# Kernel tuning notes

Hardware: AMD Instinct MI355X
Metric: run time of the kernel (lower is better)

## Reference

```python
import jax, jax.numpy as jnp
import numpy as np
from jax import lax

D_MODEL = 1024
D_STATE = 128
D_CONV = 4
EXPAND = 2
HEADDIM = 64
D_INNER = EXPAND * D_MODEL          # 2048
NHEADS = D_INNER // HEADDIM         # 32
D_IN_PROJ = 2 * D_INNER + 2 * D_STATE + NHEADS  # 4384 (z, xBC, dt)
CONV_CH = D_INNER + 2 * D_STATE     # 2304
CHUNK = 128
EPS = 1e-5
BATCH, SEQ = 2, 2048


def silu(x):
    return x * jax.nn.sigmoid(x)


def rmsnorm(x, w):
    return x * lax.rsqrt(jnp.mean(x * x, axis=-1, keepdims=True) + EPS) * w


def segsum(a):
    # a: (b,h,c,q) -> (b,h,c,q,q); [i,j] = sum_{j<k<=i} a_k, -inf above diag
    q = a.shape[-1]
    cs = jnp.cumsum(a, axis=-1)
    seg = cs[..., :, None] - cs[..., None, :]
    mask = jnp.tril(jnp.ones((q, q), dtype=bool))
    return jnp.where(mask, seg, -jnp.inf)


def ssd(xh, dt, A, B, C):
    # xh: (b,l,h,p), dt: (b,l,h), A: (h,), B,C: (b,l,n). Chunked SSD scan.
    b, l, h, p = xh.shape
    n = B.shape[-1]
    c = l // CHUNK
    X = (xh * dt[..., None]).reshape(b, c, CHUNK, h, p)
    Adt = (A * dt).reshape(b, c, CHUNK, h).transpose(0, 3, 1, 2)  # (b,h,c,q)
    Bc = B.reshape(b, c, CHUNK, n)
    Cc = C.reshape(b, c, CHUNK, n)
    Acs = jnp.cumsum(Adt, axis=-1)
    L = jnp.exp(segsum(Adt))  # (b,h,c,q,q) causal decay within chunk
    Y_diag = jnp.einsum('bcln,bcsn,bhcls,bcshp->bclhp', Cc, Bc, L, X)
    decay_states = jnp.exp(Acs[..., -1:] - Acs)
    states = jnp.einsum('bcln,bhcl,bclhp->bchpn', Bc, decay_states, X)
    chunk_decay = jnp.exp(Acs[..., -1])  # (b,h,c)

    def step(s, inp):
        st, cd = inp
        return s * cd[:, :, None, None] + st, s

    init = jnp.zeros((b, h, p, n), dtype=xh.dtype)
    _, prev = lax.scan(step, init,
                       (states.transpose(1, 0, 2, 3, 4), chunk_decay.transpose(2, 0, 1)))
    # prev: (c,b,h,p,n) = state at start of each chunk
    Y_off = jnp.einsum('bcln,cbhpn,bhcl->bclhp', Cc, prev, jnp.exp(Acs))
    return (Y_diag + Y_off).reshape(b, l, h, p)


def mamba2(x, in_w, conv_w, conv_b, dt_bias, A_log, D, gnorm_w, out_w):
    b, l, _ = x.shape
    zxbcdt = x @ in_w.T  # (b,l,D_IN_PROJ)
    z = zxbcdt[..., :D_INNER]
    xBC = zxbcdt[..., D_INNER:D_INNER + CONV_CH]
    dt = jax.nn.softplus(zxbcdt[..., D_INNER + CONV_CH:] + dt_bias)  # (b,l,h)
    # causal depthwise conv1d
    xp = jnp.pad(xBC, ((0, 0), (D_CONV - 1, 0), (0, 0)))
    conv = sum(xp[:, k:k + l, :] * conv_w[:, k] for k in range(D_CONV)) + conv_b
    xBC = silu(conv)
    xs = xBC[..., :D_INNER]
    B = xBC[..., D_INNER:D_INNER + D_STATE]
    C = xBC[..., D_INNER + D_STATE:]
    A = -jnp.exp(A_log)
    xh = xs.reshape(b, l, NHEADS, HEADDIM)
    y = ssd(xh, dt, A, B, C) + xh * D[None, None, :, None]
    y = y.reshape(b, l, D_INNER)
    y = rmsnorm(y * silu(z), gnorm_w)  # RMSNormGated
    return y @ out_w.T


def setup_inputs() -> dict:
    key = jax.random.key(0)
    ks = jax.random.split(key, 24)
    d = {}
    d['x'] = jax.random.normal(ks[0], (BATCH, SEQ, D_MODEL), dtype=jnp.float32)
    d['norm_w'] = jnp.ones((D_MODEL,), jnp.float32)
    d['out_w_blk'] = jax.random.normal(ks[1], (D_MODEL, 2 * D_MODEL), jnp.float32) * 0.02
    d['out_b_blk'] = jnp.zeros((D_MODEL,), jnp.float32)
    for i, pfx in enumerate(['f_', 'b_']):
        o = 2 + i * 10
        d[pfx + 'in_w'] = jax.random.normal(ks[o], (D_IN_PROJ, D_MODEL), jnp.float32) * 0.02
        d[pfx + 'conv_w'] = jax.random.normal(ks[o + 1], (CONV_CH, D_CONV), jnp.float32) * 0.2
        d[pfx + 'conv_b'] = jnp.zeros((CONV_CH,), jnp.float32)
        d[pfx + 'dt_bias'] = jax.random.normal(ks[o + 2], (NHEADS,), jnp.float32) * 0.1
        d[pfx + 'A_log'] = jnp.log(jax.random.uniform(ks[o + 3], (NHEADS,), jnp.float32, 1.0, 16.0))
        d[pfx + 'D'] = jnp.ones((NHEADS,), jnp.float32)
        d[pfx + 'gnorm_w'] = jnp.ones((D_INNER,), jnp.float32)
        d[pfx + 'out_w'] = jax.random.normal(ks[o + 4], (D_MODEL, D_INNER), jnp.float32) * 0.02
    return d


def reference(x, norm_w, out_w_blk, out_b_blk,
              f_in_w, f_conv_w, f_conv_b, f_dt_bias, f_A_log, f_D, f_gnorm_w, f_out_w,
              b_in_w, b_conv_w, b_conv_b, b_dt_bias, b_A_log, b_D, b_gnorm_w, b_out_w):
    xn = rmsnorm(x, norm_w)
    y_fwd = mamba2(xn, f_in_w, f_conv_w, f_conv_b, f_dt_bias, f_A_log, f_D, f_gnorm_w, f_out_w)
    y_bwd = jnp.flip(
        mamba2(jnp.flip(xn, axis=1), b_in_w, b_conv_w, b_conv_b, b_dt_bias, b_A_log, b_D, b_gnorm_w, b_out_w),
        axis=1)
    out = jnp.concatenate([y_fwd, y_bwd], axis=-1) @ out_w_blk.T + out_b_blk
    return x + out
```

## Files before the change

### kernel.cpp

```cpp
#include <hip/hip_runtime.h>
#include <hip/hip_bf16.h>
#include <math.h>

#define BATCH 2
#define SEQL 2048
#define T 4096
#define DMODEL 1024
#define DINNER 2048
#define DSTATE 128
#define NH 32
#define HD 64
#define DPROJ2 4352
#define CONVCH 2304
#define NCH 16
#define CHUNK 128
#define EPS 1e-5f

#define N_INW ((size_t)DPROJ2 * DMODEL)
#define N_OUTW ((size_t)DMODEL * DINNER)
#define N_ST ((size_t)BATCH * NCH * NH * HD * DSTATE)

typedef unsigned short u16;
typedef __bf16 bf16x8 __attribute__((ext_vector_type(8)));
typedef float f32x4 __attribute__((ext_vector_type(4)));

__device__ __forceinline__ u16 f2b(float f) {
    union { float f; unsigned u; } v; v.f = f;
    unsigned r = v.u + 0x7fffu + ((v.u >> 16) & 1u);
    return (u16)(r >> 16);
}
__device__ __forceinline__ float b2f(u16 b) {
    union { unsigned u; float f; } v; v.u = ((unsigned)b) << 16;
    return v.f;
}
__device__ __forceinline__ int flipseq(int r) {
    return (r & ~(SEQL - 1)) | ((SEQL - 1) - (r & (SEQL - 1)));
}
__device__ __forceinline__ void gload16(const u16* g, u16* l) {
    __builtin_amdgcn_global_load_lds(
        (const __attribute__((address_space(1))) void*)g,
        (__attribute__((address_space(3))) void*)l, 16, 0, 0);
}

__device__ __forceinline__ float blockReduceSum(float v) {
    __shared__ float red_[4];
    for (int off = 32; off > 0; off >>= 1) v += __shfl_down(v, off);
    int lane = threadIdx.x & 63, wid = threadIdx.x >> 6;
    if (lane == 0) red_[wid] = v;
    __syncthreads();
    if (threadIdx.x == 0) {
        float s = 0.f;
        int nw = blockDim.x >> 6;
        for (int i = 0; i < nw; ++i) s += red_[i];
        red_[0] = s;
    }
    __syncthreads();
    return red_[0];
}

__global__ __launch_bounds__(256) void k_rmsnorm(
    const float* __restrict__ x, const float* __restrict__ w,
    u16* __restrict__ outb)
{
    int row = blockIdx.x;
    const float* xr = x + (size_t)row * DMODEL;
    float ss = 0.f;
    for (int i = threadIdx.x; i < DMODEL; i += 256) { float v = xr[i]; ss += v * v; }
    float tot = blockReduceSum(ss);
    float sc = rsqrtf(tot / DMODEL + EPS);
    for (int i = threadIdx.x; i < DMODEL; i += 256)
        outb[(size_t)row * DMODEL + i] = f2b(xr[i] * sc * w[i]);
}

__global__ void k_f2b_all(
    const float* __restrict__ s0, const float* __restrict__ s1,
    const float* __restrict__ s4,
    u16* __restrict__ d_inwb, u16* __restrict__ d_owbb)
{
    size_t i = ((size_t)blockIdx.x * 256 + threadIdx.x) * 4;
    const float* s; u16* d; size_t off;
    if (i < 2 * N_INW) {
        int dir = i >= N_INW;
        off = i - (size_t)dir * N_INW;
        s = dir ? s1 : s0; d = d_inwb + (size_t)dir * N_INW;
    } else {
        off = i - 2 * N_INW;
        if (off >= N_OUTW) return;
        s = s4; d = d_owbb;
    }
    float4 v = *(const float4*)(s + off);
    ushort4 o;
    o.x = f2b(v.x); o.y = f2b(v.y); o.z = f2b(v.z); o.w = f2b(v.w);
    *(ushort4*)(d + off) = o;
}

__global__ __launch_bounds__(256) void k_tw(
    const float* __restrict__ fw, const float* __restrict__ bw, u16* __restrict__ dst)
{
    int dir = blockIdx.z;
    const float* src = dir ? bw : fw;
    u16* d = dst + (size_t)dir * N_OUTW;
    __shared__ u16 t[64][65];
    int e0 = blockIdx.y * 64, c0 = blockIdx.x * 64;
    for (int i = threadIdx.x; i < 64 * 16; i += 256) {
        int el = i >> 4, c4 = (i & 15) * 4;
        float4 v = *(const float4*)(src + (size_t)(e0 + el) * DINNER + c0 + c4);
        t[c4 + 0][el] = f2b(v.x); t[c4 + 1][el] = f2b(v.y);
        t[c4 + 2][el] = f2b(v.z); t[c4 + 3][el] = f2b(v.w);
    }
    __syncthreads();
    for (int i = threadIdx.x; i < 64 * 16; i += 256) {
        int cl = i >> 4, e4 = (i & 15) * 4;
        ushort4 o;
        o.x = t[cl][e4]; o.y = t[cl][e4 + 1]; o.z = t[cl][e4 + 2]; o.w = t[cl][e4 + 3];
        *(ushort4*)(d + (size_t)(c0 + cl) * DMODEL + e0 + e4) = o;
    }
}

__global__ __launch_bounds__(256, 4) void k_mm_in(
    const u16* __restrict__ A, const u16* __restrict__ W0,
    u16* __restrict__ zb0, u16* __restrict__ xbcraw0)
{
    const int K = DMODEL;
    int dir = blockIdx.z;
    const u16* W = W0 + (size_t)dir * N_INW;
    int m0 = blockIdx.y * 128, n0 = blockIdx.x * 128;

    u16* Cout;
    int ldcc, nbase;
    if (n0 < DINNER) {
        Cout = zb0 + (size_t)dir * T * DINNER;
        ldcc = DINNER;
        nbase = n0;
    } else {
        Cout = xbcraw0 + (size_t)dir * T * CONVCH;
        ldcc = CONVCH;
        nbase = n0 - DINNER;
    }

    __shared__ u16 As[2 * 128 * 32];
    __shared__ u16 Bs[2 * 128 * 32];
    int tid = threadIdx.x;
    int lane = tid & 63;
    int wrow = ((tid >> 6) & 1) * 64, wcol = (tid >> 7) * 64;

    int srow = tid >> 2, skof = (tid & 3) * 8;
    int ar1 = m0 + srow, ar2 = ar1 + 64;
    if (dir) { ar1 = flipseq(ar1); ar2 = flipseq(ar2); }
    const u16* ga1 = A + (size_t)ar1 * K + skof;
    const u16* ga2 = A + (size_t)ar2 * K + skof;
    const u16* gb1 = W + (size_t)(n0 + srow) * K + skof;
    const u16* gb2 = gb1 + (size_t)64 * K;
    u16* la1 = As + tid * 8;
    u16* la2 = As + 2048 + tid * 8;
    u16* lb1 = Bs + tid * 8;
    u16* lb2 = Bs + 2048 + tid * 8;

    int aoff[4], boff[4];
    #pragma unroll
    for (int i = 0; i < 4; ++i) {
        aoff[i] = (wrow + i * 16 + (lane & 15)) * 32 + ((lane >> 4) * 8);
        boff[i] = (wcol + i * 16 + (lane & 15)) * 32 + ((lane >> 4) * 8);
    }

    f32x4 acc[4][4] = {};
    for (int kt = 0; kt < K; kt += 64) {
        gload16(ga1, la1);        gload16(ga2, la2);
        gload16(ga1 + 32, la1 + 4096); gload16(ga2 + 32, la2 + 4096);
        gload16(gb1, lb1);        gload16(gb2, lb2);
        gload16(gb1 + 32, lb1 + 4096); gload16(gb2 + 32, lb2 + 4096);
        ga1 += 64; ga2 += 64; gb1 += 64; gb2 += 64;
        __syncthreads();
        #pragma unroll
        for (int ks = 0; ks < 2; ++ks) {
            bf16x8 af[4], bfv[4];
            #pragma unroll
            for (int i = 0; i < 4; ++i) af[i] = *(const bf16x8*)(As + ks * 4096 + aoff[i]);
            #pragma unroll
            for (int j = 0; j < 4; ++j) bfv[j] = *(const bf16x8*)(Bs + ks * 4096 + boff[j]);
            #pragma unroll
            for (int i = 0; i < 4; ++i)
                #pragma unroll
                for (int j = 0; j < 4; ++j)
                    acc[i][j] = __builtin_amdgcn_mfma_f32_16x16x32_bf16(af[i], bfv[j], acc[i][j], 0, 0, 0);
        }
        __syncthreads();
    }

    int rbase = m0 + wrow + ((lane >> 4) << 2);
    int cbase = nbase + wcol + (lane & 15);
    #pragma unroll
    for (int i = 0; i < 4; ++i)
        #pragma unroll
        for (int j = 0; j < 4; ++j)
            #pragma unroll
            for (int r = 0; r < 4; ++r)
                Cout[(size_t)(rbase + i * 16 + r) * ldcc + cbase + j * 16] = f2b(acc[i][j][r]);
}

__global__ __launch_bounds__(256) void k_mm64(
    const u16* __restrict__ A, size_t astride, int lda,
    const u16* __restrict__ W, size_t wstride, int K,
    u16* __restrict__ Cb, int ldc, int coffStride)
{
    int dir = blockIdx.z;
    A += (size_t)dir * astride;
    W += (size_t)dir * wstride;
    int coff = dir * coffStride;

    __shared__ u16 As[2 * 64 * 32];
    __shared__ u16 Bs[2 * 64 * 32];
    int tid = threadIdx.x;
    int lane = tid & 63;
    int w = tid >> 6;
    int m0 = blockIdx.y * 64, n0 = blockIdx.x * 64;
    int wrow = (w & 1) * 32, wcol = (w >> 1) * 32;

    int srow = tid >> 2, skof = (tid & 3) * 8;
    const u16* ga = A + (size_t)(m0 + srow) * lda + skof;
    const u16* gb = W + (size_t)(n0 + srow) * K + skof;
    u16* la = As + tid * 8;
    u16* lb = Bs + tid * 8;

    int aoff[2], boff[2];
    #pragma unroll
    for (int i = 0; i < 2; ++i) {
        aoff[i] = (wrow + i * 16 + (lane & 15)) * 32 + ((lane >> 4) * 8);
        boff[i] = (wcol + i * 16 + (lane & 15)) * 32 + ((lane >> 4) * 8);
    }

    f32x4 acc[2][2] = {};
    for (int kt = 0; kt < K; kt += 64) {
        gload16(ga, la);      gload16(ga + 32, la + 2048);
        gload16(gb, lb);      gload16(gb + 32, lb + 2048);
        ga += 64; gb += 64;
        __syncthreads();
        #pragma unroll
        for (int ks = 0; ks < 2; ++ks) {
            bf16x8 af[2], bfv[2];
            #pragma unroll
            for (int i = 0; i < 2; ++i) af[i] = *(const bf16x8*)(As + ks * 2048 + aoff[i]);
            #pragma unroll
            for (int j = 0; j < 2; ++j) bfv[j] = *(const bf16x8*)(Bs + ks * 2048 + boff[j]);
            #pragma unroll
            for (int i = 0; i < 2; ++i)
                #pragma unroll
                for (int j = 0; j < 2; ++j)
                    acc[i][j] = __builtin_amdgcn_mfma_f32_16x16x32_bf16(af[i], bfv[j], acc[i][j], 0, 0, 0);
        }
        __syncthreads();
    }

    int rbase = m0 + wrow + ((lane >> 4) << 2);
    int cbase = n0 + wcol + (lane & 15);
    #pragma unroll
    for (int i = 0; i < 2; ++i)
        #pragma unroll
        for (int j = 0; j < 2; ++j)
            #pragma unroll
            for (int r = 0; r < 4; ++r)
                Cb[(size_t)(rbase + i * 16 + r) * ldc + coff + cbase + j * 16] = f2b(acc[i][j][r]);
}

__global__ __launch_bounds__(256) void k_mm_fin(
    const u16* __restrict__ A1, const u16* __restrict__ A2,
    const u16* __restrict__ W,
    float* __restrict__ out, const float* __restrict__ bias,
    const float* __restrict__ resid)
{
    __shared__ u16 As[2 * 64 * 32];
    __shared__ u16 Bs[2 * 64 * 32];
    int tid = threadIdx.x;
    int lane = tid & 63;
    int w = tid >> 6;
    int m0 = blockIdx.y * 64, n0 = blockIdx.x * 64;
    int wrow = (w & 1) * 32, wcol = (w >> 1) * 32;

    int srow = tid >> 2, skof = (tid & 3) * 8;
    const u16* ga1 = A1 + (size_t)(m0 + srow) * DINNER + skof;
    const u16* ga2 = A2 + (size_t)flipseq(m0 + srow) * DINNER + skof;
    const u16* gb = W + (size_t)(n0 + srow) * 4096 + skof;
    u16* la = As + tid * 8;
    u16* lb = Bs + tid * 8;

    int aoff[2], boff[2];
    #pragma unroll
    for (int i = 0; i < 2; ++i) {
        aoff[i] = (wrow + i * 16 + (lane & 15)) * 32 + ((lane >> 4) * 8);
        boff[i] = (wcol + i * 16 + (lane & 15)) * 32 + ((lane >> 4) * 8);
    }

    f32x4 acc[2][2] = {};
    #pragma unroll
    for (int half = 0; half < 2; ++half) {
        const u16* ga = half ? ga2 : ga1;
        for (int kt = 0; kt < DINNER; kt += 64) {
            gload16(ga, la);      gload16(ga + 32, la + 2048);
            gload16(gb, lb);      gload16(gb + 32, lb + 2048);
            ga += 64; gb += 64;
            __syncthreads();
            #pragma unroll
            for (int ks = 0; ks < 2; ++ks) {
                bf16x8 af[2], bfv[2];
                #pragma unroll
                for (int i = 0; i < 2; ++i) af[i] = *(const bf16x8*)(As + ks * 2048 + aoff[i]);
                #pragma unroll
                for (int j = 0; j < 2; ++j) bfv[j] = *(const bf16x8*)(Bs + ks * 2048 + boff[j]);
                #pragma unroll
                for (int i = 0; i < 2; ++i)
                    #pragma unroll
                    for (int j = 0; j < 2; ++j)
                        acc[i][j] = __builtin_amdgcn_mfma_f32_16x16x32_bf16(af[i], bfv[j], acc[i][j], 0, 0, 0);
            }
            __syncthreads();
        }
    }

    int rbase = m0 + wrow + ((lane >> 4) << 2);
    int cbase = n0 + wcol + (lane & 15);
    #pragma unroll
    for (int i = 0; i < 2; ++i)
        #pragma unroll
        for (int j = 0; j < 2; ++j)
            #pragma unroll
            for (int r = 0; r < 4; ++r) {
                int row = rbase + i * 16 + r, col = cbase + j * 16;
                out[(size_t)row * DMODEL + col] =
                    acc[i][j][r] + bias[col] + resid[(size_t)row * DMODEL + col];
            }
}

__global__ __launch_bounds__(256) void k_dt2(
    const u16* __restrict__ xnb,
    const float* __restrict__ inw_f, const float* __restrict__ inw_b,
    const float* __restrict__ dtb_f, const float* __restrict__ dtb_b,
    float* __restrict__ dt)
{
    int dir = blockIdx.z;
    const float* wbase = dir ? inw_b : inw_f;
    const float* dtbia = dir ? dtb_b : dtb_f;
    float* dtp = dt + (size_t)dir * T * NH;

    int r0 = blockIdx.x * 4;
    __shared__ float xs[4][1024];
    int tid = threadIdx.x;
    #pragma unroll
    for (int rr = 0; rr < 4; ++rr) {
        int src = dir ? flipseq(r0 + rr) : (r0 + rr);
        ushort4 v = *(const ushort4*)(xnb + (size_t)src * DMODEL + tid * 4);
        xs[rr][tid * 4 + 0] = b2f(v.x); xs[rr][tid * 4 + 1] = b2f(v.y);
        xs[rr][tid * 4 + 2] = b2f(v.z); xs[rr][tid * 4 + 3] = b2f(v.w);
    }
    __syncthreads();
    int h = tid >> 3, part = tid & 7;
    const float* w = wbase + (size_t)(DPROJ2 + h) * DMODEL;
    float a0 = 0.f, a1 = 0.f, a2 = 0.f, a3 = 0.f;
    for (int kk = 0; kk < 128; ++kk) {
        int k = part + (kk << 3);
        float wv = w[k];
        a0 += xs[0][k] * wv; a1 += xs[1][k] * wv;
        a2 += xs[2][k] * wv; a3 += xs[3][k] * wv;
    }
    #pragma unroll
    for (int off = 4; off > 0; off >>= 1) {
        a0 += __shfl_down(a0, off, 8); a1 += __shfl_down(a1, off, 8);
        a2 += __shfl_down(a2, off, 8); a3 += __shfl_down(a3, off, 8);
    }
    if (part == 0) {
        float bsh = dtbia[h];
        float vv[4] = {a0, a1, a2, a3};
        #pragma unroll
        for (int rr = 0; rr < 4; ++rr) {
            float v = vv[rr] + bsh;
            dtp[(size_t)(r0 + rr) * NH + h] = (v > 20.f) ? v : log1pf(expf(v));
        }
    }
}

__global__ void k_conv(const u16* __restrict__ xraw0,
                       const float* __restrict__ cw_f, const float* __restrict__ cw_b,
                       const float* __restrict__ cb_f, const float* __restrict__ cb_b,
                       const float* __restrict__ dt0,
                       u16* __restrict__ xbcb0, u16* __restrict__ xdtb0)
{
    int dir = blockIdx.z;
    const u16* xraw = xraw0 + (size_t)dir * T * CONVCH;
    const float* cw = dir ? cw_b : cw_f;
    const float* cb = dir ? cb_b : cb_f;
    const float* dt = dt0 + (size_t)dir * T * NH;
    u16* xbcb = xbcb0 + (size_t)dir * T * CONVCH;
    u16* xdtb = xdtb0 + (size_t)dir * T * DINNER;

    int idx = blockIdx.x * blockDim.x + threadIdx.x;
    if (idx >= T * (CONVCH / 8)) return;
    int r = idx / (CONVCH / 8);
    int c8 = (idx - r * (CONVCH / 8)) * 8;
    int t = r & (SEQL - 1);
    int b0 = r - t;
    float4 cwv[8];
    #pragma unroll
    for (int j = 0; j < 8; ++j) cwv[j] = *(const float4*)(cw + (size_t)(c8 + j) * 4);
    float acc[8];
    {
        float4 c0 = *(const float4*)(cb + c8);
        float4 c1 = *(const float4*)(cb + c8 + 4);
        acc[0] = c0.x; acc[1] = c0.y; acc[2] = c0.z; acc[3] = c0.w;
        acc[4] = c1.x; acc[5] = c1.y; acc[6] = c1.z; acc[7] = c1.w;
    }
    #pragma unroll
    for (int k = 0; k < 4; ++k) {
        int tt = t + k - 3;
        if (tt < 0) continue;
        const u16* src = xraw + (size_t)(b0 + tt) * CONVCH + c8;
        ushort4 v0 = *(const ushort4*)src;
        ushort4 v1 = *(const ushort4*)(src + 4);
        float xv[8] = {b2f(v0.x), b2f(v0.y), b2f(v0.z), b2f(v0.w),
                       b2f(v1.x), b2f(v1.y), b2f(v1.z), b2f(v1.w)};
        #pragma unroll
        for (int j = 0; j < 8; ++j) {
            float wv = (k == 0) ? cwv[j].x : (k == 1) ? cwv[j].y : (k == 2) ? cwv[j].z : cwv[j].w;
            acc[j] += xv[j] * wv;
        }
    }
    ushort4 o0, o1;
    float s[8];
    #pragma unroll
    for (int j = 0; j < 8; ++j) s[j] = acc[j] / (1.f + __expf(-acc[j]));
    o0.x = f2b(s[0]); o0.y = f2b(s[1]); o0.z = f2b(s[2]); o0.w = f2b(s[3]);
    o1.x = f2b(s[4]); o1.y = f2b(s[5]); o1.z = f2b(s[6]); o1.w = f2b(s[7]);
    *(ushort4*)(xbcb + (size_t)r * CONVCH + c8) = o0;
    *(ushort4*)(xbcb + (size_t)r * CONVCH + c8 + 4) = o1;
    if (c8 < DINNER) {
        float dv = dt[(size_t)r * NH + (c8 >> 6)];
        ushort4 d0, d1;
        d0.x = f2b(s[0] * dv); d0.y = f2b(s[1] * dv); d0.z = f2b(s[2] * dv); d0.w = f2b(s[3] * dv);
        d1.x = f2b(s[4] * dv); d1.y = f2b(s[5] * dv); d1.z = f2b(s[6] * dv); d1.w = f2b(s[7] * dv);
        *(ushort4*)(xdtb + (size_t)r * DINNER + c8) = d0;
        *(ushort4*)(xdtb + (size_t)r * DINNER + c8 + 4) = d1;
    }
}

__global__ void k_acs(const float* __restrict__ dt0,
                      const float* __restrict__ Alog_f, const float* __restrict__ Alog_b,
                      float* __restrict__ acs0, float* __restrict__ cd0)
{
    int dir = blockIdx.z;
    const float* dt = dt0 + (size_t)dir * T * NH;
    const float* A_log = dir ? Alog_b : Alog_f;
    float* acs = acs0 + (size_t)dir * BATCH * NH * NCH * CHUNK;
    float* cd = cd0 + (size_t)dir * BATCH * NH * NCH;

    int bid = blockIdx.x;
    int c = bid & 15;
    int bh = bid >> 4;
    int h = bh & 31;
    int b = bh >> 5;
    int l = threadIdx.x;
    __shared__ float s[128];
    float Ah = -expf(A_log[h]);
    int r = b * SEQL + c * CHUNK + l;
    s[l] = Ah * dt[(size_t)r * NH + h];
    __syncthreads();
    for (int off = 1; off < 128; off <<= 1) {
        float t = (l >= off) ? s[l - off] : 0.f;
        __syncthreads();
        s[l] += t;
        __syncthreads();
    }
    acs[(size_t)bid * 128 + l] = s[l];
    if (l == 127) cd[bid] = expf(s[127]);
}

#define LDW 136
__global__ __launch_bounds__(256) void k_states(
    const u16* __restrict__ xbcb0, const u16* __restrict__ xdtb0,
    const float* __restrict__ acs0, u16* __restrict__ st0)
{
    int dir = blockIdx.z;
    const u16* xbcb = xbcb0 + (size_t)dir * T * CONVCH;
    const u16* xdtb = xdtb0 + (size_t)dir * T * DINNER;
    const float* acs = acs0 + (size_t)dir * BATCH * NH * NCH * CHUNK;
    u16* st = st0 + (size_t)dir * N_ST;

    __shared__ u16 Bt[128 * LDW];
    __shared__ u16 Xt[64 * LDW];
    __shared__ float acs_s[128];
    __shared__ float dec_s[128];
    int tid = threadIdx.x;
    int lane = tid & 63;
    int w = tid >> 6;
    int h = blockIdx.x & 31;
    int bc = blockIdx.x >> 5;
    int c = bc & 15, b = bc >> 4;
    int row0 = b * SEQL + c * CHUNK;

    if (tid < 128)
        acs_s[tid] = acs[(((size_t)(b * NH + h) * NCH + c) << 7) + tid];
    for (int i = tid; i < 128 * 16; i += 256) {
        int l = i >> 4, pg = (i & 15) * 4;
        ushort4 v = *(const ushort4*)(xdtb + (size_t)(row0 + l) * DINNER + h * HD + pg);
        Xt[(pg + 0) * LDW + l] = v.x; Xt[(pg + 1) * LDW + l] = v.y;
        Xt[(pg + 2) * LDW + l] = v.z; Xt[(pg + 3) * LDW + l] = v.w;
    }
    __syncthreads();
    float a_last = acs_s[127];
    if (tid < 128) dec_s[tid] = __expf(a_last - acs_s[tid]);
    __syncthreads();
    for (int i = tid; i < 128 * 32; i += 256) {
        int l = i >> 5, ng = (i & 31) * 4;
        ushort4 v = *(const ushort4*)(xbcb + (size_t)(row0 + l) * CONVCH + DINNER + ng);
        float d = dec_s[l];
        Bt[(ng + 0) * LDW + l] = f2b(b2f(v.x) * d);
        Bt[(ng + 1) * LDW + l] = f2b(b2f(v.y) * d);
        Bt[(ng + 2) * LDW + l] = f2b(b2f(v.z) * d);
        Bt[(ng + 3) * LDW + l] = f2b(b2f(v.w) * d);
    }
    __syncthreads();
    f32x4 tacc[8] = {};
    for (int kk = 0; kk < 4; ++kk) {
        bf16x8 afs = *(const bf16x8*)(Xt + (w * 16 + (lane & 15)) * LDW
                                      + kk * 32 + (lane >> 4) * 8);
        #pragma unroll
        for (int j = 0; j < 8; ++j) {
            bf16x8 bfs = *(const bf16x8*)(Bt + (j * 16 + (lane & 15)) * LDW
                                          + kk * 32 + (lane >> 4) * 8);
            tacc[j] = __builtin_amdgcn_mfma_f32_16x16x32_bf16(afs, bfs, tacc[j], 0, 0, 0);
        }
    }
    size_t sb = (size_t)blockIdx.x * (HD * DSTATE);
    #pragma unroll
    for (int j = 0; j < 8; ++j)
        #pragma unroll
        for (int r = 0; r < 4; ++r) {
            int p = w * 16 + (lane >> 4) * 4 + r;
            int n = j * 16 + (lane & 15);
            st[sb + (size_t)p * DSTATE + n] = f2b(tacc[j][r]);
        }
}

__global__ void k_scan(u16* __restrict__ st0, const float* __restrict__ cd0)
{
    int i = blockIdx.x * blockDim.x + threadIdx.x;
    if (i >= 2 * BATCH * NH * HD * DSTATE) return;
    int dir = i >> 19;
    int j = i & ((1 << 19) - 1);
    u16* st = st0 + (size_t)dir * N_ST;
    const float* cd = cd0 + (size_t)dir * BATCH * NH * NCH;
    int n = j & 127;
    int rest = j >> 7;
    int p = rest & 63; rest >>= 6;
    int h = rest & 31;
    int b = rest >> 5;
    float s = 0.f;
    for (int c = 0; c < NCH; ++c) {
        size_t idx = ((size_t)((b * NCH + c) * NH + h) * HD + p) * DSTATE + n;
        float v = b2f(st[idx]);
        st[idx] = f2b(s);
        s = s * cd[(b * NH + h) * NCH + c] + v;
    }
}

__global__ __launch_bounds__(256) void k_chunk(
    const u16* __restrict__ xbcb0, const u16* __restrict__ xdtb0,
    const float* __restrict__ acs0, const u16* __restrict__ prev0,
    const float* __restrict__ D_f, const float* __restrict__ D_b,
    u16* __restrict__ y0)
{
    int dir = blockIdx.z;
    const u16* xbcb = xbcb0 + (size_t)dir * T * CONVCH;
    const u16* xdtb = xdtb0 + (size_t)dir * T * DINNER;
    const float* acs = acs0 + (size_t)dir * BATCH * NH * NCH * CHUNK;
    const u16* prev = prev0 + (size_t)dir * N_ST;
    const float* Dp = dir ? D_b : D_f;
    u16* y = y0 + (size_t)dir * T * DINNER;

    __shared__ u16 S0[128 * LDW];
    __shared__ u16 Xt[64 * LDW];
    __shared__ float acs_s[128];
    int tid = threadIdx.x;
    int lane = tid & 63;
    int w = tid >> 6;
    int h = blockIdx.x & 31;
    int bc = blockIdx.x >> 5;
    int c = bc & 15, b = bc >> 4;
    int row0 = b * SEQL + c * CHUNK;

    if (tid < 128)
        acs_s[tid] = acs[(((size_t)(b * NH + h) * NCH + c) << 7) + tid];
    for (int i = tid; i < 128 * 16; i += 256) {
        int s = i >> 4, m8 = (i & 15) * 8;
        *(uint4*)(S0 + s * LDW + m8) =
            *(const uint4*)(xbcb + (size_t)(row0 + s) * CONVCH + DINNER + m8);
    }
    for (int i = tid; i < 128 * 16; i += 256) {
        int l = i >> 4, pg = (i & 15) * 4;
        ushort4 v = *(const ushort4*)(xdtb + (size_t)(row0 + l) * DINNER + h * HD + pg);
        Xt[(pg + 0) * LDW + l] = v.x; Xt[(pg + 1) * LDW + l] = v.y;
        Xt[(pg + 2) * LDW + l] = v.z; Xt[(pg + 3) * LDW + l] = v.w;
    }
    __syncthreads();

    int wrow = (w & 1) * 64, wcol = (w >> 1) * 64;
    const u16* cbase = xbcb + (size_t)row0 * CONVCH + DINNER + DSTATE;
    f32x4 sacc[4][4] = {};
    for (int kk = 0; kk < 4; ++kk) {
        bf16x8 af[4], bfr[4];
        #pragma unroll
        for (int i = 0; i < 4; ++i)
            af[i] = *(const bf16x8*)(cbase + (size_t)(wrow + i * 16 + (lane & 15)) * CONVCH
                                     + kk * 32 + (lane >> 4) * 8);
        #pragma unroll
        for (int j = 0; j < 4; ++j)
            bfr[j] = *(const bf16x8*)(S0 + (wcol + j * 16 + (lane & 15)) * LDW
                                      + kk * 32 + (lane >> 4) * 8);
        #pragma unroll
        for (int i = 0; i < 4; ++i)
            #pragma unroll
            for (int j = 0; j < 4; ++j)
                if (wcol + j * 16 <= wrow + i * 16 + 15)
                    sacc[i][j] = __builtin_amdgcn_mfma_f32_16x16x32_bf16(af[i], bfr[j], sacc[i][j], 0, 0, 0);
    }
    __syncthreads();
    #pragma unroll
    for (int i = 0; i < 4; ++i)
        #pragma unroll
        for (int j = 0; j < 4; ++j) {
            int s = wcol + j * 16 + (lane & 15);
            #pragma unroll
            for (int r = 0; r < 4; ++r) {
                int l = wrow + i * 16 + (lane >> 4) * 4 + r;
                float v = (s <= l) ? sacc[i][j][r] * __expf(acs_s[l] - acs_s[s]) : 0.f;
                S0[l * LDW + s] = f2b(v);
            }
        }
    __syncthreads();
    f32x4 yacc[2][4] = {};
    for (int kk = 0; kk < 4; ++kk) {
        bf16x8 af[2], bfr[4];
        #pragma unroll
        for (int i = 0; i < 2; ++i)
            af[i] = *(const bf16x8*)(S0 + (w * 32 + i * 16 + (lane & 15)) * LDW
                                     + kk * 32 + (lane >> 4) * 8);
        #pragma unroll
        for (int j = 0; j < 4; ++j)
            bfr[j] = *(const bf16x8*)(Xt + (j * 16 + (lane & 15)) * LDW
                                      + kk * 32 + (lane >> 4) * 8);
        #pragma unroll
        for (int i = 0; i < 2; ++i)
            #pragma unroll
            for (int j = 0; j < 4; ++j)
                yacc[i][j] = __builtin_amdgcn_mfma_f32_16x16x32_bf16(af[i], bfr[j], yacc[i][j], 0, 0, 0);
    }
    __syncthreads();
    size_t sb = (size_t)blockIdx.x * (HD * DSTATE);
    for (int i = tid; i < 64 * 16; i += 256) {
        int p = i >> 4, m8 = (i & 15) * 8;
        *(uint4*)(S0 + p * LDW + m8) = *(const uint4*)(prev + sb + (size_t)p * DSTATE + m8);
    }
    __syncthreads();
    f32x4 oacc[2][4] = {};
    for (int kk = 0; kk < 4; ++kk) {
        bf16x8 af[2], bfr[4];
        #pragma unroll
        for (int i = 0; i < 2; ++i)
            af[i] = *(const bf16x8*)(cbase + (size_t)(w * 32 + i * 16 + (lane & 15)) * CONVCH
                                     + kk * 32 + (lane >> 4) * 8);
        #pragma unroll
        for (int j = 0; j < 4; ++j)
            bfr[j] = *(const bf16x8*)(S0 + (j * 16 + (lane & 15)) * LDW
                                      + kk * 32 + (lane >> 4) * 8);
        #pragma unroll
        for (int i = 0; i < 2; ++i)
            #pragma unroll
            for (int j = 0; j < 4; ++j)
                oacc[i][j] = __builtin_amdgcn_mfma_f32_16x16x32_bf16(af[i], bfr[j], oacc[i][j], 0, 0, 0);
    }
    float Dh = Dp[h];
    #pragma unroll
    for (int i = 0; i < 2; ++i)
        #pragma unroll
        for (int j = 0; j < 4; ++j)
            #pragma unroll
            for (int r = 0; r < 4; ++r) {
                int l = w * 32 + i * 16 + (lane >> 4) * 4 + r;
                int p = j * 16 + (lane & 15);
                float val = yacc[i][j][r] + __expf(acs_s[l]) * oacc[i][j][r]
                          + b2f(xbcb[(size_t)(row0 + l) * CONVCH + h * HD + p]) * Dh;
                y[(size_t)(row0 + l) * DINNER + h * HD + p] = f2b(val);
            }
}

__global__ __launch_bounds__(256) void k_gate(
    const u16* __restrict__ y0, const u16* __restrict__ zb0,
    const float* __restrict__ gw_f, const float* __restrict__ gw_b,
    u16* __restrict__ out0)
{
    int dir = blockIdx.z;
    const u16* y = y0 + (size_t)dir * T * DINNER;
    const u16* zb = zb0 + (size_t)dir * T * DINNER;
    const float* gw = dir ? gw_b : gw_f;
    u16* out = out0 + (size_t)dir * T * DINNER;

    int r = blockIdx.x;
    __shared__ float tbuf[DINNER];
    int tid = threadIdx.x;
    float ss = 0.f;
    #pragma unroll
    for (int it = 0; it < 2; ++it) {
        int i = (it * 256 + tid) * 4;
        ushort4 yv = *(const ushort4*)(y + (size_t)r * DINNER + i);
        ushort4 zv = *(const ushort4*)(zb + (size_t)r * DINNER + i);
        float z0 = b2f(zv.x), z1 = b2f(zv.y), z2 = b2f(zv.z), z3 = b2f(zv.w);
        float t0 = b2f(yv.x) * (z0 / (1.f + __expf(-z0)));
        float t1 = b2f(yv.y) * (z1 / (1.f + __expf(-z1)));
        float t2 = b2f(yv.z) * (z2 / (1.f + __expf(-z2)));
        float t3 = b2f(yv.w) * (z3 / (1.f + __expf(-z3)));
        tbuf[i] = t0; tbuf[i + 1] = t1; tbuf[i + 2] = t2; tbuf[i + 3] = t3;
        ss += t0 * t0 + t1 * t1 + t2 * t2 + t3 * t3;
    }
    float tot = blockReduceSum(ss);
    float sc = rsqrtf(tot / DINNER + EPS);
    #pragma unroll
    for (int it = 0; it < 2; ++it) {
        int i = (it * 256 + tid) * 4;
        ushort4 o;
        o.x = f2b(tbuf[i] * sc * gw[i]);
        o.y = f2b(tbuf[i + 1] * sc * gw[i + 1]);
        o.z = f2b(tbuf[i + 2] * sc * gw[i + 2]);
        o.w = f2b(tbuf[i + 3] * sc * gw[i + 3]);
        *(ushort4*)(out + (size_t)r * DINNER + i) = o;
    }
}

extern "C" void kernel_launch(void* const* d_in, const int* in_sizes, int n_in,
                              void* d_out, int out_size, void* d_ws, size_t ws_size,
                              hipStream_t stream)
{
    const float* x         = (const float*)d_in[0];
    const float* norm_w    = (const float*)d_in[1];
    const float* out_w_blk = (const float*)d_in[2];
    const float* out_b_blk = (const float*)d_in[3];
    const float* f_in_w    = (const float*)d_in[4];
    const float* f_conv_w  = (const float*)d_in[5];
    const float* f_conv_b  = (const float*)d_in[6];
    const float* f_dt_bias = (const float*)d_in[7];
    const float* f_A_log   = (const float*)d_in[8];
    const float* f_D       = (const float*)d_in[9];
    const float* f_gnorm_w = (const float*)d_in[10];
    const float* f_out_w   = (const float*)d_in[11];
    const float* b_in_w    = (const float*)d_in[12];
    const float* b_conv_w  = (const float*)d_in[13];
    const float* b_conv_b  = (const float*)d_in[14];
    const float* b_dt_bias = (const float*)d_in[15];
    const float* b_A_log   = (const float*)d_in[16];
    const float* b_D       = (const float*)d_in[17];
    const float* b_gnorm_w = (const float*)d_in[18];
    const float* b_out_w   = (const float*)d_in[19];
    float* out = (float*)d_out;

    char* ws = (char*)d_ws;
    u16*  xnb    = (u16*)ws;   ws += (size_t)T * DMODEL * 2;
    u16*  zb     = (u16*)ws;   ws += (size_t)2 * T * DINNER * 2;
    u16*  xbcraw = (u16*)ws;   ws += (size_t)2 * T * CONVCH * 2;
    u16*  xbcb   = (u16*)ws;   ws += (size_t)2 * T * CONVCH * 2;
    u16*  xdtb   = (u16*)ws;   ws += (size_t)2 * T * DINNER * 2;
    float* dtb   = (float*)ws; ws += (size_t)2 * T * NH * 4;
    float* acs   = (float*)ws; ws += (size_t)2 * BATCH * NH * NCH * CHUNK * 4;
    float* cd    = (float*)ws; ws += (size_t)2 * BATCH * NH * NCH * 4;
    u16*  stb    = (u16*)ws;   ws += (size_t)2 * N_ST * 2;
    u16*  inwb   = (u16*)ws;   ws += (size_t)2 * N_INW * 2;
    u16*  fowT2  = (u16*)ws;   ws += (size_t)2 * N_OUTW * 2;
    u16*  owbb   = (u16*)ws;   ws += (size_t)N_OUTW * 2;
    u16*  yb16  = xbcraw;
    u16*  ybb   = xdtb;
    u16*  Mcomb = xbcb;

    k_rmsnorm<<<T, 256, 0, stream>>>(x, norm_w, xnb);
    {
        size_t tot = 2 * N_INW + N_OUTW;
        int blocks = (int)((tot / 4 + 255) / 256);
        k_f2b_all<<<blocks, 256, 0, stream>>>(f_in_w, b_in_w, out_w_blk, inwb, owbb);
    }
    {
        dim3 g(DINNER / 64, DMODEL / 64, 2);
        k_tw<<<g, 256, 0, stream>>>(f_out_w, b_out_w, fowT2);
    }

    {
        dim3 g(DPROJ2 / 128, T / 128, 2);
        k_mm_in<<<g, 256, 0, stream>>>(xnb, inwb, zb, xbcraw);
    }
    {
        dim3 g(T / 4, 1, 2);
        k_dt2<<<g, 256, 0, stream>>>(xnb, f_in_w, b_in_w, f_dt_bias, b_dt_bias, dtb);
    }
    {
        dim3 g((T * (CONVCH / 8) + 255) / 256, 1, 2);
        k_conv<<<g, 256, 0, stream>>>(xbcraw, f_conv_w, b_conv_w, f_conv_b, b_conv_b,
                                      dtb, xbcb, xdtb);
    }
    {
        dim3 g(BATCH * NH * NCH, 1, 2);
        k_acs<<<g, 128, 0, stream>>>(dtb, f_A_log, b_A_log, acs, cd);
    }
    {
        dim3 g(BATCH * NCH * NH, 1, 2);
        k_states<<<g, 256, 0, stream>>>(xbcb, xdtb, acs, stb);
    }
    k_scan<<<(2 * BATCH * NH * HD * DSTATE) / 256, 256, 0, stream>>>(stb, cd);
    {
        dim3 g(BATCH * NCH * NH, 1, 2);
        k_chunk<<<g, 256, 0, stream>>>(xbcb, xdtb, acs, stb, f_D, b_D, yb16);
    }
    {
        dim3 g(T, 1, 2);
        k_gate<<<g, 256, 0, stream>>>(yb16, zb, f_gnorm_w, b_gnorm_w, ybb);
    }
    {
        dim3 g(DINNER / 64, DMODEL / 64, 2);
        k_mm64<<<g, 256, 0, stream>>>(owbb, (size_t)DMODEL, DINNER,
                                      fowT2, N_OUTW, DMODEL,
                                      Mcomb, 2 * DINNER, DINNER);
    }
    {
        dim3 g(DMODEL / 64, T / 64, 1);
        k_mm_fin<<<g, 256, 0, stream>>>(ybb, ybb + (size_t)T * DINNER, Mcomb,
                                        out, out_b_blk, x);
    }
}
```

Before: 587.6 us.

## Merge weight-prep kernels, fold chunk cumsum into states, restructure final GEMM loop

Combines the bf16 weight conversion and the out-projection transpose into one launch, and moves the per-chunk A*dt cumsum into the states kernel so the separate k_acs launch goes away. The final GEMM now loads both direction halves per K-step with doubled shared buffers, which halves the barrier count. The gate kernel keeps values in registers instead of a shared buffer. The aim is fewer launches and less synchronisation overhead, at the cost of more shared memory in the final GEMM and a redundant scan in k_states.

```diff
diff --git a/kernel.cpp b/kernel.cpp
--- a/kernel.cpp
+++ b/kernel.cpp
@@ -19,6 +19,8 @@
 #define N_INW ((size_t)DPROJ2 * DMODEL)
 #define N_OUTW ((size_t)DMODEL * DINNER)
 #define N_ST ((size_t)BATCH * NCH * NH * HD * DSTATE)
+#define F2B_BLOCKS 10752
+#define TW_BLOCKS 1024
 
 typedef unsigned short u16;
 typedef __bf16 bf16x8 __attribute__((ext_vector_type(8)));
@@ -72,36 +74,38 @@
         outb[(size_t)row * DMODEL + i] = f2b(xr[i] * sc * w[i]);
 }
 
-__global__ void k_f2b_all(
-    const float* __restrict__ s0, const float* __restrict__ s1,
-    const float* __restrict__ s4,
-    u16* __restrict__ d_inwb, u16* __restrict__ d_owbb)
-{
-    size_t i = ((size_t)blockIdx.x * 256 + threadIdx.x) * 4;
-    const float* s; u16* d; size_t off;
-    if (i < 2 * N_INW) {
-        int dir = i >= N_INW;
-        off = i - (size_t)dir * N_INW;
-        s = dir ? s1 : s0; d = d_inwb + (size_t)dir * N_INW;
-    } else {
-        off = i - 2 * N_INW;
-        if (off >= N_OUTW) return;
-        s = s4; d = d_owbb;
-    }
-    float4 v = *(const float4*)(s + off);
-    ushort4 o;
-    o.x = f2b(v.x); o.y = f2b(v.y); o.z = f2b(v.z); o.w = f2b(v.w);
-    *(ushort4*)(d + off) = o;
-}
-
-__global__ __launch_bounds__(256) void k_tw(
-    const float* __restrict__ fw, const float* __restrict__ bw, u16* __restrict__ dst)
-{
-    int dir = blockIdx.z;
-    const float* src = dir ? bw : fw;
-    u16* d = dst + (size_t)dir * N_OUTW;
+__global__ __launch_bounds__(256) void k_wprep(
+    const float* __restrict__ f_in_w, const float* __restrict__ b_in_w,
+    const float* __restrict__ out_w_blk,
+    const float* __restrict__ f_out_w, const float* __restrict__ b_out_w,
+    u16* __restrict__ d_inwb, u16* __restrict__ d_owbb, u16* __restrict__ d_fowT)
+{
     __shared__ u16 t[64][65];
-    int e0 = blockIdx.y * 64, c0 = blockIdx.x * 64;
+    int bid = blockIdx.x;
+    if (bid < F2B_BLOCKS) {
+        size_t i = ((size_t)bid * 256 + threadIdx.x) * 4;
+        const float* s; u16* d; size_t off;
+        if (i < 2 * N_INW) {
+            int dir = i >= N_INW;
+            off = i - (size_t)dir * N_INW;
+            s = dir ? b_in_w : f_in_w; d = d_inwb + (size_t)dir * N_INW;
+        } else {
+            off = i - 2 * N_INW;
+            if (off >= N_OUTW) return;
+            s = out_w_blk; d = d_owbb;
+        }
+        float4 v = *(const float4*)(s + off);
+        ushort4 o;
+        o.x = f2b(v.x); o.y = f2b(v.y); o.z = f2b(v.z); o.w = f2b(v.w);
+        *(ushort4*)(d + off) = o;
+        return;
+    }
+    int b2 = bid - F2B_BLOCKS;
+    int dir = b2 >> 9;
+    int rem = b2 & 511;
+    int c0 = (rem & 31) * 64, e0 = (rem >> 5) * 64;
+    const float* src = dir ? b_out_w : f_out_w;
+    u16* d = d_fowT + (size_t)dir * N_OUTW;
     for (int i = threadIdx.x; i < 64 * 16; i += 256) {
         int el = i >> 4, c4 = (i & 15) * 4;
         float4 v = *(const float4*)(src + (size_t)(e0 + el) * DINNER + c0 + c4);
@@ -268,8 +272,8 @@
     float* __restrict__ out, const float* __restrict__ bias,
     const float* __restrict__ resid)
 {
-    __shared__ u16 As[2 * 64 * 32];
-    __shared__ u16 Bs[2 * 64 * 32];
+    __shared__ u16 As[4 * 64 * 32];
+    __shared__ u16 Bs[4 * 64 * 32];
     int tid = threadIdx.x;
     int lane = tid & 63;
     int w = tid >> 6;
@@ -279,7 +283,8 @@
     int srow = tid >> 2, skof = (tid & 3) * 8;
     const u16* ga1 = A1 + (size_t)(m0 + srow) * DINNER + skof;
     const u16* ga2 = A2 + (size_t)flipseq(m0 + srow) * DINNER + skof;
-    const u16* gb = W + (size_t)(n0 + srow) * 4096 + skof;
+    const u16* gb1 = W + (size_t)(n0 + srow) * 4096 + skof;
+    const u16* gb2 = gb1 + 2048;
     u16* la = As + tid * 8;
     u16* lb = Bs + tid * 8;
 
@@ -291,29 +296,32 @@
     }
 
     f32x4 acc[2][2] = {};
-    #pragma unroll
-    for (int half = 0; half < 2; ++half) {
-        const u16* ga = half ? ga2 : ga1;
-        for (int kt = 0; kt < DINNER; kt += 64) {
-            gload16(ga, la);      gload16(ga + 32, la + 2048);
-            gload16(gb, lb);      gload16(gb + 32, lb + 2048);
-            ga += 64; gb += 64;
-            __syncthreads();
+    for (int kt = 0; kt < DINNER; kt += 64) {
+        gload16(ga1, la);       gload16(ga1 + 32, la + 2048);
+        gload16(ga2, la + 4096); gload16(ga2 + 32, la + 6144);
+        gload16(gb1, lb);       gload16(gb1 + 32, lb + 2048);
+        gload16(gb2, lb + 4096); gload16(gb2 + 32, lb + 6144);
+        ga1 += 64; ga2 += 64; gb1 += 64; gb2 += 64;
+        __syncthreads();
+        #pragma unroll
+        for (int half = 0; half < 2; ++half) {
             #pragma unroll
             for (int ks = 0; ks < 2; ++ks) {
                 bf16x8 af[2], bfv[2];
                 #pragma unroll
-                for (int i = 0; i < 2; ++i) af[i] = *(const bf16x8*)(As + ks * 2048 + aoff[i]);
+                for (int i = 0; i < 2; ++i)
+                    af[i] = *(const bf16x8*)(As + half * 4096 + ks * 2048 + aoff[i]);
                 #pragma unroll
-                for (int j = 0; j < 2; ++j) bfv[j] = *(const bf16x8*)(Bs + ks * 2048 + boff[j]);
+                for (int j = 0; j < 2; ++j)
+                    bfv[j] = *(const bf16x8*)(Bs + half * 4096 + ks * 2048 + boff[j]);
                 #pragma unroll
                 for (int i = 0; i < 2; ++i)
                     #pragma unroll
                     for (int j = 0; j < 2; ++j)
                         acc[i][j] = __builtin_amdgcn_mfma_f32_16x16x32_bf16(af[i], bfv[j], acc[i][j], 0, 0, 0);
             }
-            __syncthreads();
         }
+        __syncthreads();
     }
 
     int rbase = m0 + wrow + ((lane >> 4) << 2);
@@ -440,51 +448,25 @@
     }
 }
 
-__global__ void k_acs(const float* __restrict__ dt0,
-                      const float* __restrict__ Alog_f, const float* __restrict__ Alog_b,
-                      float* __restrict__ acs0, float* __restrict__ cd0)
+#define LDW 136
+__global__ __launch_bounds__(256) void k_states(
+    const u16* __restrict__ xbcb0, const u16* __restrict__ xdtb0,
+    const float* __restrict__ dt0,
+    const float* __restrict__ Alog_f, const float* __restrict__ Alog_b,
+    float* __restrict__ acs0, float* __restrict__ cd0, u16* __restrict__ st0)
 {
     int dir = blockIdx.z;
+    const u16* xbcb = xbcb0 + (size_t)dir * T * CONVCH;
+    const u16* xdtb = xdtb0 + (size_t)dir * T * DINNER;
     const float* dt = dt0 + (size_t)dir * T * NH;
     const float* A_log = dir ? Alog_b : Alog_f;
     float* acs = acs0 + (size_t)dir * BATCH * NH * NCH * CHUNK;
     float* cd = cd0 + (size_t)dir * BATCH * NH * NCH;
-
-    int bid = blockIdx.x;
-    int c = bid & 15;
-    int bh = bid >> 4;
-    int h = bh & 31;
-    int b = bh >> 5;
-    int l = threadIdx.x;
-    __shared__ float s[128];
-    float Ah = -expf(A_log[h]);
-    int r = b * SEQL + c * CHUNK + l;
-    s[l] = Ah * dt[(size_t)r * NH + h];
-    __syncthreads();
-    for (int off = 1; off < 128; off <<= 1) {
-        float t = (l >= off) ? s[l - off] : 0.f;
-        __syncthreads();
-        s[l] += t;
-        __syncthreads();
-    }
-    acs[(size_t)bid * 128 + l] = s[l];
-    if (l == 127) cd[bid] = expf(s[127]);
-}
-
-#define LDW 136
-__global__ __launch_bounds__(256) void k_states(
-    const u16* __restrict__ xbcb0, const u16* __restrict__ xdtb0,
-    const float* __restrict__ acs0, u16* __restrict__ st0)
-{
-    int dir = blockIdx.z;
-    const u16* xbcb = xbcb0 + (size_t)dir * T * CONVCH;
-    const u16* xdtb = xdtb0 + (size_t)dir * T * DINNER;
-    const float* acs = acs0 + (size_t)dir * BATCH * NH * NCH * CHUNK;
     u16* st = st0 + (size_t)dir * N_ST;
 
     __shared__ u16 Bt[128 * LDW];
     __shared__ u16 Xt[64 * LDW];
-    __shared__ float acs_s[128];
+    __shared__ float cs[128];
     __shared__ float dec_s[128];
     int tid = threadIdx.x;
     int lane = tid & 63;
@@ -494,8 +476,10 @@
     int c = bc & 15, b = bc >> 4;
     int row0 = b * SEQL + c * CHUNK;
 
-    if (tid < 128)
-        acs_s[tid] = acs[(((size_t)(b * NH + h) * NCH + c) << 7) + tid];
+    if (tid < 128) {
+        float Ah = -expf(A_log[h]);
+        cs[tid] = Ah * dt[(size_t)(row0 + tid) * NH + h];
+    }
     for (int i = tid; i < 128 * 16; i += 256) {
         int l = i >> 4, pg = (i & 15) * 4;
         ushort4 v = *(const ushort4*)(xdtb + (size_t)(row0 + l) * DINNER + h * HD + pg);
@@ -503,8 +487,18 @@
         Xt[(pg + 2) * LDW + l] = v.z; Xt[(pg + 3) * LDW + l] = v.w;
     }
     __syncthreads();
-    float a_last = acs_s[127];
-    if (tid < 128) dec_s[tid] = __expf(a_last - acs_s[tid]);
+    for (int off = 1; off < 128; off <<= 1) {
+        float tval = 0.f;
+        if (tid < 128 && tid >= off) tval = cs[tid - off];
+        __syncthreads();
+        if (tid < 128) cs[tid] += tval;
+        __syncthreads();
+    }
+    size_t abase = ((size_t)(b * NH + h) * NCH + c) << 7;
+    if (tid < 128) acs[abase + tid] = cs[tid];
+    float a_last = cs[127];
+    if (tid == 127) cd[(b * NH + h) * NCH + c] = expf(a_last);
+    if (tid < 128) dec_s[tid] = __expf(a_last - cs[tid]);
     __syncthreads();
     for (int i = tid; i < 128 * 32; i += 256) {
         int l = i >> 5, ng = (i & 31) * 4;
@@ -702,8 +696,8 @@
     u16* out = out0 + (size_t)dir * T * DINNER;
 
     int r = blockIdx.x;
-    __shared__ float tbuf[DINNER];
     int tid = threadIdx.x;
+    float tv[8];
     float ss = 0.f;
     #pragma unroll
     for (int it = 0; it < 2; ++it) {
@@ -715,7 +709,7 @@
         float t1 = b2f(yv.y) * (z1 / (1.f + __expf(-z1)));
         float t2 = b2f(yv.z) * (z2 / (1.f + __expf(-z2)));
         float t3 = b2f(yv.w) * (z3 / (1.f + __expf(-z3)));
-        tbuf[i] = t0; tbuf[i + 1] = t1; tbuf[i + 2] = t2; tbuf[i + 3] = t3;
+        tv[it * 4 + 0] = t0; tv[it * 4 + 1] = t1; tv[it * 4 + 2] = t2; tv[it * 4 + 3] = t3;
         ss += t0 * t0 + t1 * t1 + t2 * t2 + t3 * t3;
     }
     float tot = blockReduceSum(ss);
@@ -724,10 +718,10 @@
     for (int it = 0; it < 2; ++it) {
         int i = (it * 256 + tid) * 4;
         ushort4 o;
-        o.x = f2b(tbuf[i] * sc * gw[i]);
-        o.y = f2b(tbuf[i + 1] * sc * gw[i + 1]);
-        o.z = f2b(tbuf[i + 2] * sc * gw[i + 2]);
-        o.w = f2b(tbuf[i + 3] * sc * gw[i + 3]);
+        o.x = f2b(tv[it * 4 + 0] * sc * gw[i]);
+        o.y = f2b(tv[it * 4 + 1] * sc * gw[i + 1]);
+        o.z = f2b(tv[it * 4 + 2] * sc * gw[i + 2]);
+        o.w = f2b(tv[it * 4 + 3] * sc * gw[i + 3]);
         *(ushort4*)(out + (size_t)r * DINNER + i) = o;
     }
 }
@@ -776,15 +770,8 @@
     u16*  Mcomb = xbcb;
 
     k_rmsnorm<<<T, 256, 0, stream>>>(x, norm_w, xnb);
-    {
-        size_t tot = 2 * N_INW + N_OUTW;
-        int blocks = (int)((tot / 4 + 255) / 256);
-        k_f2b_all<<<blocks, 256, 0, stream>>>(f_in_w, b_in_w, out_w_blk, inwb, owbb);
-    }
-    {
-        dim3 g(DINNER / 64, DMODEL / 64, 2);
-        k_tw<<<g, 256, 0, stream>>>(f_out_w, b_out_w, fowT2);
-    }
+    k_wprep<<<F2B_BLOCKS + TW_BLOCKS, 256, 0, stream>>>(
+        f_in_w, b_in_w, out_w_blk, f_out_w, b_out_w, inwb, owbb, fowT2);
 
     {
         dim3 g(DPROJ2 / 128, T / 128, 2);
@@ -800,12 +787,8 @@
                                       dtb, xbcb, xdtb);
     }
     {
-        dim3 g(BATCH * NH * NCH, 1, 2);
-        k_acs<<<g, 128, 0, stream>>>(dtb, f_A_log, b_A_log, acs, cd);
-    }
-    {
         dim3 g(BATCH * NCH * NH, 1, 2);
-        k_states<<<g, 256, 0, stream>>>(xbcb, xdtb, acs, stb);
+        k_states<<<g, 256, 0, stream>>>(xbcb, xdtb, dtb, f_A_log, b_A_log, acs, cd, stb);
     }
     k_scan<<<(2 * BATCH * NH * HD * DSTATE) / 256, 256, 0, stream>>>(stb, cd);
     {
```

Result: no change. 591.2 us (+0.6%).
